# Optimization experiments

Hardware: AMD Instinct MI355X
Metric: run time of the kernel (lower is better)

The kernel has to match this reference:

```python
import math
import jax, jax.numpy as jnp
import numpy as np

N_HEADS = 16
D_MODEL = 1024
USER_DIM = 512
D_K = D_MODEL // N_HEADS


def _linear_params(key, fan_in, fan_out):
    k1, k2 = jax.random.split(key)
    bound = 1.0 / math.sqrt(fan_in)
    W = jax.random.uniform(k1, (fan_in, fan_out), minval=-bound, maxval=bound, dtype=jnp.float32)
    b = jax.random.uniform(k2, (fan_out,), minval=-bound, maxval=bound, dtype=jnp.float32)
    return W, b


def setup_inputs() -> dict:
    key = jax.random.key(0)
    ks = jax.random.split(key, 7)
    B, S, Skv = 4, 2048, 2048
    query = jax.random.normal(ks[0], (B, S, D_MODEL), dtype=jnp.float32)
    k_in = jax.random.normal(ks[1], (B, Skv, USER_DIM), dtype=jnp.float32)
    v_in = jax.random.normal(ks[2], (B, Skv, USER_DIM), dtype=jnp.float32)
    Wq, bq = _linear_params(ks[3], D_MODEL, D_MODEL)
    Wk, bk = _linear_params(ks[4], USER_DIM, D_MODEL)
    Wv, bv = _linear_params(ks[5], USER_DIM, D_MODEL)
    Wo, bo = _linear_params(ks[6], D_MODEL, D_MODEL)
    return {"query": query, "key": k_in, "value": v_in,
            "Wq": Wq, "bq": bq, "Wk": Wk, "bk": bk,
            "Wv": Wv, "bv": bv, "Wo": Wo, "bo": bo}


def reference(query, key, value, Wq, bq, Wk, bk, Wv, bv, Wo, bo):
    B, S, _ = query.shape
    # zero-padding masks: rows whose raw features sum to exactly 0
    mask_key = (jnp.sum(key, axis=-1, keepdims=True) == 0)      # [B,Skv,1]
    mask_value = (jnp.sum(value, axis=-1, keepdims=True) == 0)  # [B,Skv,1]

    q = (query @ Wq + bq).reshape(B, S, N_HEADS, D_K).transpose(0, 2, 1, 3)   # [B,H,S,Dk]
    k = key @ Wk + bk
    k = jnp.where(mask_key, 0.0, k).reshape(B, -1, N_HEADS, D_K).transpose(0, 2, 1, 3)
    v = value @ Wv + bv
    v = jnp.where(mask_value, 0.0, v).reshape(B, -1, N_HEADS, D_K).transpose(0, 2, 1, 3)

    scores = jnp.einsum('bhqd,bhkd->bhqk', q, k) / math.sqrt(D_K)  # [B,H,S,Skv]
    p_attn = jax.nn.softmax(scores, axis=-1)
    # dropout is identity in eval/reference mode
    attn = jnp.einsum('bhqk,bhkd->bhqd', p_attn, v)                # [B,H,S,Dk]
    attn = attn.transpose(0, 2, 1, 3).reshape(B, S, N_HEADS * D_K)
    return attn @ Wo + bo
```

## Files before the change

kernel.cpp:

```cpp
#include <hip/hip_runtime.h>
#include <hip/hip_bf16.h>

typedef __attribute__((ext_vector_type(8))) short bf16x8;
typedef __attribute__((ext_vector_type(4))) float floatx4;
typedef __attribute__((ext_vector_type(16))) float floatx16;
typedef __attribute__((ext_vector_type(4))) unsigned short u16x4;
typedef __attribute__((ext_vector_type(4))) int intx4;

#define MFMA16(a, b, c) __builtin_amdgcn_mfma_f32_16x16x32_bf16(a, b, c, 0, 0, 0)
#define MFMA32(a, b, c) __builtin_amdgcn_mfma_f32_32x32x16_bf16(a, b, c, 0, 0, 0)

__device__ __forceinline__ unsigned short f2bf(float f) {
  unsigned int u = __float_as_uint(f);
  u += 0x7fffu + ((u >> 16) & 1u);
  return (unsigned short)(u >> 16);
}

__device__ __forceinline__ unsigned int pkbf2(float lo, float hi) {
  __hip_bfloat162 h = __float22bfloat162_rn(float2{lo, hi});
  unsigned int r;
  __builtin_memcpy(&r, &h, 4);
  return r;
}

__device__ __forceinline__ void gll16(const void* g, void* l) {
  __builtin_amdgcn_global_load_lds(
      (const __attribute__((address_space(1))) void*)g,
      (__attribute__((address_space(3))) void*)l, 16, 0, 0);
}

__global__ __launch_bounds__(256) void cvt_all_kernel(
    const float* __restrict__ query, const float* __restrict__ key,
    const float* __restrict__ value, unsigned short* __restrict__ qbf,
    unsigned short* __restrict__ kbf, unsigned short* __restrict__ vbf,
    float* __restrict__ maskK, float* __restrict__ maskV) {
  const int bx = blockIdx.x;
  if (bx < 8192) {
    int i = bx * 256 + threadIdx.x;
    floatx4 v = ((const floatx4*)query)[i];
    u16x4 o;
    o[0] = f2bf(v[0]); o[1] = f2bf(v[1]); o[2] = f2bf(v[2]); o[3] = f2bf(v[3]);
    ((u16x4*)qbf)[i] = o;
    return;
  }
  const int mb = bx - 8192;
  const float* src = (mb < 2048) ? key : value;
  unsigned short* dst = (mb < 2048) ? kbf : vbf;
  float* mask = (mb < 2048) ? maskK : maskV;
  const int blk = mb & 2047;
  const int w = threadIdx.x >> 6, l = threadIdx.x & 63;
  const size_t row = (size_t)blk * 4 + w;
  const float* s = src + row * 512;
  float v[8]; float sum = 0.f;
#pragma unroll
  for (int i = 0; i < 8; ++i) { v[i] = s[l + i * 64]; sum += v[i]; }
#pragma unroll
  for (int d = 1; d < 64; d <<= 1) sum += __shfl_xor(sum, d, 64);
  if (l == 0) mask[row] = (sum == 0.0f) ? 0.f : 1.f;
  unsigned short* dr = dst + row * 512;
#pragma unroll
  for (int i = 0; i < 8; ++i) dr[l + i * 64] = f2bf(v[i]);
}

__global__ __launch_bounds__(256) void wtt_all_kernel(
    const float* __restrict__ W0, const float* __restrict__ W1,
    const float* __restrict__ W2, const float* __restrict__ W3,
    unsigned short* __restrict__ D0, unsigned short* __restrict__ D1,
    unsigned short* __restrict__ D2, unsigned short* __restrict__ D3,
    float scale0) {
  const int z = blockIdx.z;
  const int K = (z == 0 || z == 3) ? 1024 : 512;
  if (blockIdx.y * 32 >= K) return;
  const float* W = (z == 0) ? W0 : (z == 1) ? W1 : (z == 2) ? W2 : W3;
  unsigned short* Wt = (z == 0) ? D0 : (z == 1) ? D1 : (z == 2) ? D2 : D3;
  const float scale = (z == 0) ? scale0 : 1.0f;
  __shared__ float tile[32][33];
  const int tx = threadIdx.x, ty = threadIdx.y;
  const int n_ = blockIdx.x * 32 + tx;
  const int k0 = blockIdx.y * 32;
#pragma unroll
  for (int i = ty; i < 32; i += 8) tile[i][tx] = W[(size_t)(k0 + i) * 1024 + n_];
  __syncthreads();
  const int k_ = k0 + tx;
#pragma unroll
  for (int i = ty; i < 32; i += 8)
    Wt[(size_t)(blockIdx.x * 32 + i) * K + k_] = f2bf(tile[tx][i] * scale);
}

template <int MASKF, int VT, int OF32>
__device__ __forceinline__ void gemm_body(
    const unsigned short* __restrict__ A, const unsigned short* __restrict__ Bt,
    const float* __restrict__ bias, const float* __restrict__ mask,
    void* __restrict__ outp, int N, int K, float bscale,
    unsigned short (&As)[2][128 * 32], unsigned short (&Bs)[2][128 * 32],
    int m_tile, int n_tile) {
  const int t = threadIdx.x;
  const int w = t >> 6, l = t & 63, g = l >> 4, lm = l & 15;
  const int m0 = m_tile * 128, n0 = n_tile * 128;
  const int wm = w >> 1, wn = w & 1;
  floatx4 acc[4][4] = {};

  const int NK = K >> 5;
  auto stage = [&](int kt, int buf) {
#pragma unroll
    for (int issue = 0; issue < 2; ++issue) {
      const int tt = issue * 256 + t;
      gll16(A + (size_t)(m0 + (tt >> 2)) * K + kt * 32 + (tt & 3) * 8,
            (void*)((char*)&As[buf][0] + issue * 4096 + w * 1024));
      gll16(Bt + (size_t)(n0 + (tt >> 2)) * K + kt * 32 + (tt & 3) * 8,
            (void*)((char*)&Bs[buf][0] + issue * 4096 + w * 1024));
    }
  };

  stage(0, 0);
  int cur = 0;
  for (int kt = 0; kt < NK; ++kt) {
    __syncthreads();
    if (kt + 1 < NK) stage(kt + 1, cur ^ 1);
    const unsigned short* Ab = &As[cur][0];
    const unsigned short* Bb = &Bs[cur][0];
    bf16x8 af[4], bfr[4];
#pragma unroll
    for (int mr = 0; mr < 4; ++mr)
      af[mr] = *(const bf16x8*)(Ab + (wm * 64 + mr * 16 + lm) * 32 + g * 8);
#pragma unroll
    for (int nf = 0; nf < 4; ++nf)
      bfr[nf] = *(const bf16x8*)(Bb + (wn * 64 + nf * 16 + lm) * 32 + g * 8);
#pragma unroll
    for (int mr = 0; mr < 4; ++mr)
#pragma unroll
      for (int nf = 0; nf < 4; ++nf)
        acc[mr][nf] = MFMA16(af[mr], bfr[nf], acc[mr][nf]);
    cur ^= 1;
  }

#pragma unroll
  for (int nf = 0; nf < 4; ++nf) {
    const int n = n0 + wn * 64 + nf * 16 + lm;
    const float bv = bias[n] * bscale;
#pragma unroll
    for (int mr = 0; mr < 4; ++mr) {
      const int mb = m0 + wm * 64 + mr * 16 + g * 4;
      if (VT) {
        u16x4 pk;
#pragma unroll
        for (int j = 0; j < 4; ++j) {
          float v = acc[mr][nf][j] + bv;
          if (MASKF) v *= mask[mb + j];
          pk[j] = f2bf(v);
        }
        const int bb = mb >> 11;
        const int s = mb & 2047;
        const int sp = (s & ~12) | ((s & 8) >> 1) | ((s & 4) << 1);
        *(u16x4*)((unsigned short*)outp + ((size_t)bb * 1024 + n) * 2048 + sp) = pk;
      } else {
#pragma unroll
        for (int j = 0; j < 4; ++j) {
          float v = acc[mr][nf][j] + bv;
          if (MASKF) v *= mask[mb + j];
          if (OF32) ((float*)outp)[(size_t)(mb + j) * N + n] = v;
          else ((unsigned short*)outp)[(size_t)(mb + j) * N + n] = f2bf(v);
        }
      }
    }
  }
}

__device__ __forceinline__ void gemm_tiles(int& m_tile, int& n_tile) {
  m_tile = (blockIdx.x << 3) | (blockIdx.y >> 3);
  n_tile = blockIdx.y & 7;
}

__global__ __launch_bounds__(256) void qkv_gemm_kernel(
    const unsigned short* __restrict__ qbf, const unsigned short* __restrict__ Wqt,
    const float* __restrict__ bq, unsigned short* __restrict__ Qp,
    const unsigned short* __restrict__ kbf, const unsigned short* __restrict__ Wkt,
    const float* __restrict__ bk, const float* __restrict__ maskK,
    unsigned short* __restrict__ Kp,
    const unsigned short* __restrict__ vbf, const unsigned short* __restrict__ Wvt,
    const float* __restrict__ bv, const float* __restrict__ maskV,
    unsigned short* __restrict__ Vtp, float QS) {
  __shared__ __align__(16) unsigned short As[2][128 * 32];
  __shared__ __align__(16) unsigned short Bs[2][128 * 32];
  int m_tile, n_tile;
  gemm_tiles(m_tile, n_tile);
  if (blockIdx.z == 0)
    gemm_body<0, 0, 0>(qbf, Wqt, bq, nullptr, Qp, 1024, 1024, QS, As, Bs, m_tile, n_tile);
  else if (blockIdx.z == 1)
    gemm_body<1, 0, 0>(kbf, Wkt, bk, maskK, Kp, 1024, 512, 1.0f, As, Bs, m_tile, n_tile);
  else
    gemm_body<1, 1, 0>(vbf, Wvt, bv, maskV, Vtp, 1024, 512, 1.0f, As, Bs, m_tile, n_tile);
}

__global__ __launch_bounds__(256) void out_gemm_kernel(
    const unsigned short* __restrict__ A, const unsigned short* __restrict__ Bt,
    const float* __restrict__ bias, float* __restrict__ outp) {
  __shared__ __align__(16) unsigned short As[2][128 * 32];
  __shared__ __align__(16) unsigned short Bs[2][128 * 32];
  int m_tile, n_tile;
  gemm_tiles(m_tile, n_tile);
  gemm_body<0, 0, 1>(A, Bt, bias, nullptr, outp, 1024, 1024, 1.0f, As, Bs, m_tile, n_tile);
}

__global__ __launch_bounds__(256, 4) void flash_kernel(
    const unsigned short* __restrict__ Qp, const unsigned short* __restrict__ Kp,
    const unsigned short* __restrict__ Vt, unsigned short* __restrict__ Ctx) {
  __shared__ __align__(16) unsigned short Ks[2][64 * 64];
  __shared__ __align__(16) unsigned short Vs[2][64 * 64];
  const int t = threadIdx.x, w = t >> 6, l = t & 63, hi = l >> 5, ln = l & 31;

  const int orig = blockIdx.y * 16 + blockIdx.x;
  const int lin = (orig & 7) * 128 + (orig >> 3);
  const int bh = lin >> 4, qt = lin & 15;
  const int b = bh >> 4, h = bh & 15;
  const int q0 = qt * 128 + w * 32;
  const size_t qg = (size_t)b * 2048 + q0;

  bf16x8 qf[4];
#pragma unroll
  for (int kc = 0; kc < 4; ++kc)
    qf[kc] = *(const bf16x8*)(Qp + (qg + ln) * 1024 + h * 64 + kc * 16 + hi * 8);

  floatx16 oacc[2] = {};
  float mx = -3.0e38f, sm = 0.f;

  const unsigned swz2 = (unsigned)((((ln & 7) ^ ((ln >> 3) & 3)) ^ hi) << 4);

  auto stage = [&](int tile, int buf) {
#pragma unroll
    for (int issue = 0; issue < 2; ++issue) {
      const int tt = issue * 256 + t;
      const int row = tt >> 3;
      const int c = (tt & 7) ^ (row & 7) ^ ((row >> 3) & 3);
      gll16(Kp + ((size_t)b * 2048 + tile * 64 + row) * 1024 + h * 64 + c * 8,
            (void*)((char*)&Ks[buf][0] + issue * 4096 + w * 1024));
      gll16(Vt + ((size_t)b * 1024 + h * 64 + row) * 2048 + tile * 64 + c * 8,
            (void*)((char*)&Vs[buf][0] + issue * 4096 + w * 1024));
    }
  };

  stage(0, 0);
  int cur = 0;
  for (int tile = 0; tile < 32; ++tile) {
    __syncthreads();
    if (tile + 1 < 32) stage(tile + 1, cur ^ 1);

    const char* Kb = (const char*)&Ks[cur][0] + (unsigned)(ln * 128) + swz2;
    const char* Vb = (const char*)&Vs[cur][0] + (unsigned)(ln * 128) + swz2;

    floatx16 sacc[2] = {};
#pragma unroll
    for (int c = 0; c < 2; ++c) {
#pragma unroll
      for (int kc = 0; kc < 4; ++kc) {
        bf16x8 kf = *(const bf16x8*)((uintptr_t)(Kb + c * 4096) ^ (unsigned)(kc * 32));
        sacc[c] = MFMA32(kf, qf[kc], sacc[c]);
      }
    }

    float a[8];
#pragma unroll
    for (int i = 0; i < 8; ++i) {
      const int cc = i >> 2, rr = (i & 3) * 4;
      a[i] = fmaxf(fmaxf(sacc[cc][rr], sacc[cc][rr + 1]),
                   fmaxf(sacc[cc][rr + 2], sacc[cc][rr + 3]));
    }
    float pm = fmaxf(fmaxf(fmaxf(a[0], a[1]), fmaxf(a[2], a[3])),
                     fmaxf(fmaxf(a[4], a[5]), fmaxf(a[6], a[7])));
    pm = fmaxf(pm, __shfl_xor(pm, 32, 64));
    if (!__all(pm - mx <= 8.f)) {
      const float mnew = fmaxf(mx, pm);
      const float corr = __builtin_amdgcn_exp2f(mx - mnew);
      mx = mnew;
      sm *= corr;
#pragma unroll
      for (int dc = 0; dc < 2; ++dc)
#pragma unroll
        for (int r = 0; r < 16; ++r) oacc[dc][r] *= corr;
    }
#pragma unroll
    for (int c = 0; c < 2; ++c)
#pragma unroll
      for (int r = 0; r < 16; ++r)
        sacc[c][r] = __builtin_amdgcn_exp2f(sacc[c][r] - mx);
    {
      float s16[16];
#pragma unroll
      for (int i = 0; i < 16; ++i) s16[i] = sacc[0][i] + sacc[1][i];
      float s8[8];
#pragma unroll
      for (int i = 0; i < 8; ++i) s8[i] = s16[i] + s16[i + 8];
      float s4[4];
#pragma unroll
      for (int i = 0; i < 4; ++i) s4[i] = s8[i] + s8[i + 4];
      float ps = (s4[0] + s4[1]) + (s4[2] + s4[3]);
      ps += __shfl_xor(ps, 32, 64);
      sm += ps;
    }

#pragma unroll
    for (int c = 0; c < 2; ++c)
#pragma unroll
      for (int h2 = 0; h2 < 2; ++h2) {
        intx4 wd;
#pragma unroll
        for (int wj = 0; wj < 4; ++wj)
          wd[wj] = (int)pkbf2(sacc[c][h2 * 8 + 2 * wj], sacc[c][h2 * 8 + 2 * wj + 1]);
        const bf16x8 pf = __builtin_bit_cast(bf16x8, wd);
#pragma unroll
        for (int dc = 0; dc < 2; ++dc) {
          bf16x8 vf = *(const bf16x8*)((uintptr_t)(Vb + dc * 4096) ^ (unsigned)(c * 64 + h2 * 32));
          oacc[dc] = MFMA32(vf, pf, oacc[dc]);
        }
      }
    cur ^= 1;
  }

  __syncthreads();
  const float inv = 1.f / sm;
  unsigned short* lds_o = &Ks[0][0] + w * 2048;
#pragma unroll
  for (int dc = 0; dc < 2; ++dc)
#pragma unroll
    for (int r = 0; r < 16; r += 2) {
      const int d = dc * 32 + (r & 3) + 8 * (r >> 2) + 4 * hi;
      const unsigned int pk = pkbf2(oacc[dc][r] * inv, oacc[dc][r + 1] * inv);
      *(unsigned int*)(&lds_o[ln * 64 + (((d >> 3) ^ (ln & 7)) * 8) + (d & 7)]) = pk;
    }
  __builtin_amdgcn_s_waitcnt(0);
#pragma unroll
  for (int i = 0; i < 4; ++i) {
    const int q = i * 8 + (l >> 3);
    const int cd = l & 7;
    bf16x8 vv = *(const bf16x8*)(&lds_o[q * 64 + ((cd ^ (q & 7)) * 8)]);
    *(bf16x8*)(&Ctx[(qg + q) * 1024 + h * 64 + cd * 8]) = vv;
  }
}

extern "C" void kernel_launch(void* const* d_in, const int* in_sizes, int n_in,
                              void* d_out, int out_size, void* d_ws, size_t ws_size,
                              hipStream_t stream) {
  const float* query = (const float*)d_in[0];
  const float* key   = (const float*)d_in[1];
  const float* value = (const float*)d_in[2];
  const float* Wq = (const float*)d_in[3];
  const float* bq = (const float*)d_in[4];
  const float* Wk = (const float*)d_in[5];
  const float* bk = (const float*)d_in[6];
  const float* Wv = (const float*)d_in[7];
  const float* bv = (const float*)d_in[8];
  const float* Wo = (const float*)d_in[9];
  const float* bo = (const float*)d_in[10];

  char* ws = (char*)d_ws;
  unsigned short* qbf = (unsigned short*)ws;  ws += (size_t)8192 * 1024 * 2;
  unsigned short* kbf = (unsigned short*)ws;  ws += (size_t)8192 * 512 * 2;
  unsigned short* vbf = (unsigned short*)ws;  ws += (size_t)8192 * 512 * 2;
  unsigned short* Wqt = (unsigned short*)ws;  ws += (size_t)1024 * 1024 * 2;
  unsigned short* Wkt = (unsigned short*)ws;  ws += (size_t)1024 * 512 * 2;
  unsigned short* Wvt = (unsigned short*)ws;  ws += (size_t)1024 * 512 * 2;
  unsigned short* Wot = (unsigned short*)ws;  ws += (size_t)1024 * 1024 * 2;
  unsigned short* Qp  = (unsigned short*)ws;  ws += (size_t)8192 * 1024 * 2;
  unsigned short* Kp  = (unsigned short*)ws;  ws += (size_t)8192 * 1024 * 2;
  unsigned short* Vtp = (unsigned short*)ws;  ws += (size_t)8192 * 1024 * 2;
  unsigned short* Ctx = (unsigned short*)ws;  ws += (size_t)8192 * 1024 * 2;
  float* maskK = (float*)ws;                  ws += (size_t)8192 * 4;
  float* maskV = (float*)ws;                  ws += (size_t)8192 * 4;

  const float QS = 0.125f * 1.44269504f;

  cvt_all_kernel<<<12288, 256, 0, stream>>>(query, key, value, qbf, kbf, vbf,
                                            maskK, maskV);
  wtt_all_kernel<<<dim3(32, 32, 4), dim3(32, 8), 0, stream>>>(
      Wq, Wk, Wv, Wo, Wqt, Wkt, Wvt, Wot, QS);

  qkv_gemm_kernel<<<dim3(8, 64, 3), 256, 0, stream>>>(
      qbf, Wqt, bq, Qp, kbf, Wkt, bk, maskK, Kp, vbf, Wvt, bv, maskV, Vtp, QS);

  flash_kernel<<<dim3(16, 64), 256, 0, stream>>>(Qp, Kp, Vtp, Ctx);

  out_gemm_kernel<<<dim3(8, 64), 256, 0, stream>>>(Ctx, Wot, bo, (float*)d_out);
}
```

Before: 212.8 us.

## Software-pipeline QK^T one tile ahead in flash kernel and merge prep kernels

```diff
diff --git a/kernel.cpp b/kernel.cpp
--- a/kernel.cpp
+++ b/kernel.cpp
@@ -29,11 +29,16 @@
       (__attribute__((address_space(3))) void*)l, 16, 0, 0);
 }
 
-__global__ __launch_bounds__(256) void cvt_all_kernel(
+__global__ __launch_bounds__(256) void prep_kernel(
     const float* __restrict__ query, const float* __restrict__ key,
     const float* __restrict__ value, unsigned short* __restrict__ qbf,
     unsigned short* __restrict__ kbf, unsigned short* __restrict__ vbf,
-    float* __restrict__ maskK, float* __restrict__ maskV) {
+    float* __restrict__ maskK, float* __restrict__ maskV,
+    const float* __restrict__ W0, const float* __restrict__ W1,
+    const float* __restrict__ W2, const float* __restrict__ W3,
+    unsigned short* __restrict__ D0, unsigned short* __restrict__ D1,
+    unsigned short* __restrict__ D2, unsigned short* __restrict__ D3,
+    float scale0) {
   const int bx = blockIdx.x;
   if (bx < 8192) {
     int i = bx * 256 + threadIdx.x;
@@ -43,48 +48,45 @@
     ((u16x4*)qbf)[i] = o;
     return;
   }
-  const int mb = bx - 8192;
-  const float* src = (mb < 2048) ? key : value;
-  unsigned short* dst = (mb < 2048) ? kbf : vbf;
-  float* mask = (mb < 2048) ? maskK : maskV;
-  const int blk = mb & 2047;
-  const int w = threadIdx.x >> 6, l = threadIdx.x & 63;
-  const size_t row = (size_t)blk * 4 + w;
-  const float* s = src + row * 512;
-  float v[8]; float sum = 0.f;
-#pragma unroll
-  for (int i = 0; i < 8; ++i) { v[i] = s[l + i * 64]; sum += v[i]; }
-#pragma unroll
-  for (int d = 1; d < 64; d <<= 1) sum += __shfl_xor(sum, d, 64);
-  if (l == 0) mask[row] = (sum == 0.0f) ? 0.f : 1.f;
-  unsigned short* dr = dst + row * 512;
-#pragma unroll
-  for (int i = 0; i < 8; ++i) dr[l + i * 64] = f2bf(v[i]);
-}
-
-__global__ __launch_bounds__(256) void wtt_all_kernel(
-    const float* __restrict__ W0, const float* __restrict__ W1,
-    const float* __restrict__ W2, const float* __restrict__ W3,
-    unsigned short* __restrict__ D0, unsigned short* __restrict__ D1,
-    unsigned short* __restrict__ D2, unsigned short* __restrict__ D3,
-    float scale0) {
-  const int z = blockIdx.z;
+  if (bx < 12288) {
+    const int mb = bx - 8192;
+    const float* src = (mb < 2048) ? key : value;
+    unsigned short* dst = (mb < 2048) ? kbf : vbf;
+    float* mask = (mb < 2048) ? maskK : maskV;
+    const int blk = mb & 2047;
+    const int w = threadIdx.x >> 6, l = threadIdx.x & 63;
+    const size_t row = (size_t)blk * 4 + w;
+    const float* s = src + row * 512;
+    float v[8]; float sum = 0.f;
+#pragma unroll
+    for (int i = 0; i < 8; ++i) { v[i] = s[l + i * 64]; sum += v[i]; }
+#pragma unroll
+    for (int d = 1; d < 64; d <<= 1) sum += __shfl_xor(sum, d, 64);
+    if (l == 0) mask[row] = (sum == 0.0f) ? 0.f : 1.f;
+    unsigned short* dr = dst + row * 512;
+#pragma unroll
+    for (int i = 0; i < 8; ++i) dr[l + i * 64] = f2bf(v[i]);
+    return;
+  }
+  const int idx = bx - 12288;
+  const int z = idx >> 10;
+  const int ky = (idx >> 5) & 31, kx = idx & 31;
   const int K = (z == 0 || z == 3) ? 1024 : 512;
-  if (blockIdx.y * 32 >= K) return;
+  if (ky * 32 >= K) return;
   const float* W = (z == 0) ? W0 : (z == 1) ? W1 : (z == 2) ? W2 : W3;
   unsigned short* Wt = (z == 0) ? D0 : (z == 1) ? D1 : (z == 2) ? D2 : D3;
   const float scale = (z == 0) ? scale0 : 1.0f;
   __shared__ float tile[32][33];
-  const int tx = threadIdx.x, ty = threadIdx.y;
-  const int n_ = blockIdx.x * 32 + tx;
-  const int k0 = blockIdx.y * 32;
+  const int tx = threadIdx.x & 31, ty = threadIdx.x >> 5;
+  const int n_ = kx * 32 + tx;
+  const int k0 = ky * 32;
 #pragma unroll
   for (int i = ty; i < 32; i += 8) tile[i][tx] = W[(size_t)(k0 + i) * 1024 + n_];
   __syncthreads();
   const int k_ = k0 + tx;
 #pragma unroll
   for (int i = ty; i < 32; i += 8)
-    Wt[(size_t)(blockIdx.x * 32 + i) * K + k_] = f2bf(tile[tx][i] * scale);
+    Wt[(size_t)(kx * 32 + i) * K + k_] = f2bf(tile[tx][i] * scale);
 }
 
 template <int MASKF, int VT, int OF32>
@@ -205,9 +207,9 @@
 __global__ __launch_bounds__(256, 4) void flash_kernel(
     const unsigned short* __restrict__ Qp, const unsigned short* __restrict__ Kp,
     const unsigned short* __restrict__ Vt, unsigned short* __restrict__ Ctx) {
-  __shared__ __align__(16) unsigned short Ks[2][64 * 64];
+  __shared__ __align__(16) unsigned short Ks[3][64 * 64];
   __shared__ __align__(16) unsigned short Vs[2][64 * 64];
-  const int t = threadIdx.x, w = t >> 6, l = t & 63, hi = l >> 5, ln = l & 31;
+  const int t0 = threadIdx.x, w = t0 >> 6, l = t0 & 63, hi = l >> 5, ln = l & 31;
 
   const int orig = blockIdx.y * 16 + blockIdx.x;
   const int lin = (orig & 7) * 128 + (orig >> 3);
@@ -226,44 +228,53 @@
 
   const unsigned swz2 = (unsigned)((((ln & 7) ^ ((ln >> 3) & 3)) ^ hi) << 4);
 
-  auto stage = [&](int tile, int buf) {
+  auto stageK = [&](int tile, int buf) {
 #pragma unroll
     for (int issue = 0; issue < 2; ++issue) {
-      const int tt = issue * 256 + t;
+      const int tt = issue * 256 + t0;
       const int row = tt >> 3;
       const int c = (tt & 7) ^ (row & 7) ^ ((row >> 3) & 3);
       gll16(Kp + ((size_t)b * 2048 + tile * 64 + row) * 1024 + h * 64 + c * 8,
-            (void*)((char*)&Ks[buf][0] + issue * 4096 + w * 1024));
+            (void*)((char*)&Ks[0][0] + buf * 8192 + issue * 4096 + w * 1024));
+    }
+  };
+  auto stageV = [&](int tile, int buf) {
+#pragma unroll
+    for (int issue = 0; issue < 2; ++issue) {
+      const int tt = issue * 256 + t0;
+      const int row = tt >> 3;
+      const int c = (tt & 7) ^ (row & 7) ^ ((row >> 3) & 3);
       gll16(Vt + ((size_t)b * 1024 + h * 64 + row) * 2048 + tile * 64 + c * 8,
-            (void*)((char*)&Vs[buf][0] + issue * 4096 + w * 1024));
+            (void*)((char*)&Vs[0][0] + buf * 8192 + issue * 4096 + w * 1024));
     }
   };
 
-  stage(0, 0);
-  int cur = 0;
-  for (int tile = 0; tile < 32; ++tile) {
-    __syncthreads();
-    if (tile + 1 < 32) stage(tile + 1, cur ^ 1);
-
-    const char* Kb = (const char*)&Ks[cur][0] + (unsigned)(ln * 128) + swz2;
-    const char* Vb = (const char*)&Vs[cur][0] + (unsigned)(ln * 128) + swz2;
-
-    floatx16 sacc[2] = {};
-#pragma unroll
-    for (int c = 0; c < 2; ++c) {
+  auto qk = [&](int tile, int buf, floatx16 (&sW)[2]) {
+    const char* Kb = (const char*)&Ks[0][0] + buf * 8192 + (unsigned)(ln * 128) + swz2;
+    sW[0] = (floatx16)0.f;
+    sW[1] = (floatx16)0.f;
+#pragma unroll
+    for (int c = 0; c < 2; ++c)
 #pragma unroll
       for (int kc = 0; kc < 4; ++kc) {
         bf16x8 kf = *(const bf16x8*)((uintptr_t)(Kb + c * 4096) ^ (unsigned)(kc * 32));
-        sacc[c] = MFMA32(kf, qf[kc], sacc[c]);
+        sW[c] = MFMA32(kf, qf[kc], sW[c]);
       }
+  };
+
+  auto body = [&](int t, floatx16 (&sR)[2], floatx16 (&sW)[2]) {
+    if (t + 2 < 32) stageK(t + 2, (t + 2) % 3);
+    if (t + 1 < 32) {
+      stageV(t + 1, (t + 1) & 1);
+      qk(t + 1, (t + 1) % 3, sW);
     }
 
     float a[8];
 #pragma unroll
     for (int i = 0; i < 8; ++i) {
       const int cc = i >> 2, rr = (i & 3) * 4;
-      a[i] = fmaxf(fmaxf(sacc[cc][rr], sacc[cc][rr + 1]),
-                   fmaxf(sacc[cc][rr + 2], sacc[cc][rr + 3]));
+      a[i] = fmaxf(fmaxf(sR[cc][rr], sR[cc][rr + 1]),
+                   fmaxf(sR[cc][rr + 2], sR[cc][rr + 3]));
     }
     float pm = fmaxf(fmaxf(fmaxf(a[0], a[1]), fmaxf(a[2], a[3])),
                      fmaxf(fmaxf(a[4], a[5]), fmaxf(a[6], a[7])));
@@ -282,11 +293,11 @@
     for (int c = 0; c < 2; ++c)
 #pragma unroll
       for (int r = 0; r < 16; ++r)
-        sacc[c][r] = __builtin_amdgcn_exp2f(sacc[c][r] - mx);
+        sR[c][r] = __builtin_amdgcn_exp2f(sR[c][r] - mx);
     {
       float s16[16];
 #pragma unroll
-      for (int i = 0; i < 16; ++i) s16[i] = sacc[0][i] + sacc[1][i];
+      for (int i = 0; i < 16; ++i) s16[i] = sR[0][i] + sR[1][i];
       float s8[8];
 #pragma unroll
       for (int i = 0; i < 8; ++i) s8[i] = s16[i] + s16[i + 8];
@@ -298,6 +309,7 @@
       sm += ps;
     }
 
+    const char* Vb = (const char*)&Vs[0][0] + (t & 1) * 8192 + (unsigned)(ln * 128) + swz2;
 #pragma unroll
     for (int c = 0; c < 2; ++c)
 #pragma unroll
@@ -305,7 +317,7 @@
         intx4 wd;
 #pragma unroll
         for (int wj = 0; wj < 4; ++wj)
-          wd[wj] = (int)pkbf2(sacc[c][h2 * 8 + 2 * wj], sacc[c][h2 * 8 + 2 * wj + 1]);
+          wd[wj] = (int)pkbf2(sR[c][h2 * 8 + 2 * wj], sR[c][h2 * 8 + 2 * wj + 1]);
         const bf16x8 pf = __builtin_bit_cast(bf16x8, wd);
 #pragma unroll
         for (int dc = 0; dc < 2; ++dc) {
@@ -313,10 +325,21 @@
           oacc[dc] = MFMA32(vf, pf, oacc[dc]);
         }
       }
-    cur ^= 1;
-  }
-
+    __syncthreads();
+  };
+
+  stageK(0, 0);
+  stageV(0, 0);
+  stageK(1, 1);
   __syncthreads();
+  floatx16 sA[2], sB[2];
+  qk(0, 0, sA);
+
+  for (int tt = 0; tt < 16; ++tt) {
+    body(2 * tt, sA, sB);
+    body(2 * tt + 1, sB, sA);
+  }
+
   const float inv = 1.f / sm;
   unsigned short* lds_o = &Ks[0][0] + w * 2048;
 #pragma unroll
@@ -369,10 +392,9 @@
 
   const float QS = 0.125f * 1.44269504f;
 
-  cvt_all_kernel<<<12288, 256, 0, stream>>>(query, key, value, qbf, kbf, vbf,
-                                            maskK, maskV);
-  wtt_all_kernel<<<dim3(32, 32, 4), dim3(32, 8), 0, stream>>>(
-      Wq, Wk, Wv, Wo, Wqt, Wkt, Wvt, Wot, QS);
+  prep_kernel<<<16384, 256, 0, stream>>>(query, key, value, qbf, kbf, vbf,
+                                         maskK, maskV, Wq, Wk, Wv, Wo,
+                                         Wqt, Wkt, Wvt, Wot, QS);
 
   qkv_gemm_kernel<<<dim3(8, 64, 3), 256, 0, stream>>>(
       qbf, Wqt, bq, Qp, kbf, Wkt, bk, maskK, Kp, vbf, Wvt, bv, maskV, Vtp, QS);
```

New measurement: 337.1 us. +58.4%, slower.
